# Optimization experiments

Measured on AMD Instinct MI355X. Metric: run time of the kernel, lower is better.

The kernel has to match this reference:

```python
import jax, jax.numpy as jnp
import numpy as np

X_SIZE = 1024
N_HEADS = 16
N_BASIS = 10
MAX_LEN = 4096
CACHE_KEEP_LEN = 4096
B = 8
T_NEW = 128
T_PREV = 4096
HEAD_DIM = X_SIZE // N_HEADS
LN_EPS = 1e-5


def setup_inputs() -> dict:
    key = jax.random.key(0)
    ks = jax.random.split(key, 9)
    def w(k, shape, s):
        return jax.random.normal(k, shape, dtype=jnp.float32) * s
    inv = 1.0 / np.sqrt(X_SIZE)
    return {
        "X": w(ks[0], (B, T_NEW, X_SIZE), 1.0),
        "cache_K": w(ks[1], (B, T_PREV, X_SIZE), 1.0),
        "cache_V": w(ks[2], (B, T_PREV, X_SIZE), 1.0),
        "Wq": w(ks[3], (X_SIZE, X_SIZE), 0.1 * inv),   # Q_SCALE=0.1 (NormedLinear init scale)
        "bq": jnp.zeros((X_SIZE,), jnp.float32),
        "Wk": w(ks[4], (X_SIZE, X_SIZE), 0.2 * inv),   # K_SCALE=0.2, no bias
        "Wv": w(ks[5], (X_SIZE, X_SIZE), 1.0 * inv),   # V_SCALE*sqrt(scale), no bias
        "Wproj": w(ks[6], (X_SIZE, X_SIZE), 1.0 * inv),
        "bproj": jnp.zeros((X_SIZE,), jnp.float32),
        "Wr": w(ks[7], (X_SIZE, N_BASIS * N_HEADS), 0.1 * inv),  # R_SCALE=0.1
        "br": jnp.zeros((N_BASIS * N_HEADS,), jnp.float32),
        "b_nd": w(ks[8], (N_BASIS, MAX_LEN), 0.2),     # B_SCALE=0.2
        "ln_g": jnp.ones((X_SIZE,), jnp.float32),
        "ln_b": jnp.zeros((X_SIZE,), jnp.float32),
    }


def _split_heads(x, h):
    b, t, e = x.shape
    return x.reshape(b, t, h, e // h).transpose(0, 2, 1, 3).reshape(b * h, t, e // h)


def _merge_heads(x, h):
    bh, t, q = x.shape
    b = bh // h
    return x.reshape(b, h, t, q).transpose(0, 2, 1, 3).reshape(b, t, h * q)


def reference(X, cache_K, cache_V, Wq, bq, Wk, Wv, Wproj, bproj, Wr, br, b_nd, ln_g, ln_b):
    Bsz, t, E = X.shape
    # ln_x
    mu = jnp.mean(X, axis=-1, keepdims=True)
    var = jnp.var(X, axis=-1, keepdims=True)
    Xn = (X - mu) / jnp.sqrt(var + LN_EPS) * ln_g + ln_b
    # projections on new tokens
    Q = Xn @ Wq + bq
    K_new = Xn @ Wk
    V_new = Xn @ Wv
    # update_state: append cache (startfull=max(Tprev-cache_keep_len,0))
    Tprev = cache_K.shape[1]
    start = max(Tprev - CACHE_KEEP_LEN, 0)
    Kf = jnp.concatenate([cache_K[:, start:], K_new], axis=1)  # (B, T, E)
    Vf = jnp.concatenate([cache_V[:, start:], V_new], axis=1)
    T = Kf.shape[1]
    Qh = _split_heads(Q, N_HEADS)   # (B*h, t, q)
    Kh = _split_heads(Kf, N_HEADS)  # (B*h, T, q)
    Vh = _split_heads(Vf, N_HEADS)
    # relattn logits: R_btn (B*h, t, n_basis), bandified basis D_ntT
    R = _split_heads(Xn @ Wr + br, N_HEADS)
    d = (T - t + jnp.arange(t)[:, None]) - jnp.arange(T)[None, :]  # (t, T) time diff
    valid = (d >= 0) & (d < MAX_LEN)
    D = jnp.where(valid[None, :, :], b_nd[:, jnp.clip(d, 0, MAX_LEN - 1)], 0.0)  # (n, t, T)
    extra = jnp.einsum('btn,ntT->btT', R, D)  # (B*h, t, T)
    # causal band bias (mask=None -> default causal mask with maxlen window)
    bias = jnp.where(valid, 0.0, -1e9)[None, :, :]
    logits = bias + extra + jnp.einsum('btq,bTq->btT', Qh, Kh) * (1.0 / np.sqrt(HEAD_DIM))
    W_btT = jax.nn.softmax(logits, axis=-1)
    A = _merge_heads(jnp.einsum('btT,bTq->btq', W_btT, Vh), N_HEADS)  # (B, t, E)
    return X + (A @ Wproj + bproj)
```

## Files before the change

kernel.cpp:

```cpp
#include <hip/hip_runtime.h>
#include <hip/hip_bf16.h>

typedef __bf16 bf16;
typedef __bf16 bf16x8 __attribute__((ext_vector_type(8)));
typedef float f32x4 __attribute__((ext_vector_type(4)));
typedef unsigned short u16;
typedef u16 u16x4 __attribute__((ext_vector_type(4)));

#define MFMA16(a, b, c) __builtin_amdgcn_mfma_f32_16x16x32_bf16(a, b, c, 0, 0, 0)

static __device__ __forceinline__ bf16x8 cvt8(float4 a, float4 b) {
  union { bf16 h[8]; bf16x8 v; } u;
  u.h[0] = (bf16)a.x; u.h[1] = (bf16)a.y; u.h[2] = (bf16)a.z; u.h[3] = (bf16)a.w;
  u.h[4] = (bf16)b.x; u.h[5] = (bf16)b.y; u.h[6] = (bf16)b.z; u.h[7] = (bf16)b.w;
  return u.v;
}

__global__ __launch_bounds__(256) void k_ln(const float* __restrict__ X,
                                            const float* __restrict__ g,
                                            const float* __restrict__ bb,
                                            bf16* __restrict__ Xn) {
  int m = blockIdx.x, t = threadIdx.x;
  const float* row = X + (size_t)m * 1024;
  float4 x = ((const float4*)row)[t];
  float s1 = x.x + x.y + x.z + x.w;
  float s2 = x.x * x.x + x.y * x.y + x.z * x.z + x.w * x.w;
#pragma unroll
  for (int off = 1; off < 64; off <<= 1) {
    s1 += __shfl_xor(s1, off);
    s2 += __shfl_xor(s2, off);
  }
  __shared__ float ws1[4], ws2[4];
  int w = t >> 6;
  if ((t & 63) == 0) { ws1[w] = s1; ws2[w] = s2; }
  __syncthreads();
  s1 = ws1[0] + ws1[1] + ws1[2] + ws1[3];
  s2 = ws2[0] + ws2[1] + ws2[2] + ws2[3];
  float mu = s1 * (1.f / 1024.f);
  float var = s2 * (1.f / 1024.f) - mu * mu;
  float rstd = rsqrtf(var + 1e-5f);
  float4 gg = ((const float4*)g)[t];
  float4 bv = ((const float4*)bb)[t];
  union { bf16 h[4]; u16x4 v; } u;
  u.h[0] = (bf16)((x.x - mu) * rstd * gg.x + bv.x);
  u.h[1] = (bf16)((x.y - mu) * rstd * gg.y + bv.y);
  u.h[2] = (bf16)((x.z - mu) * rstd * gg.z + bv.z);
  u.h[3] = (bf16)((x.w - mu) * rstd * gg.w + bv.w);
  ((u16x4*)(Xn + (size_t)m * 1024))[t] = u.v;
}

__global__ __launch_bounds__(256) void k_convert(const float* __restrict__ Wq,
                                                 const float* __restrict__ Wk,
                                                 const float* __restrict__ Wv,
                                                 const float* __restrict__ Wr,
                                                 const float* __restrict__ Wp,
                                                 bf16* __restrict__ Wt_all,
                                                 bf16* __restrict__ Wpt) {
  __shared__ float tile[64][65];
  int t = threadIdx.x;
  int bn = blockIdx.x / 16, bk = blockIdx.x % 16;
  int n0 = bn * 64, k0 = bk * 64;
#pragma unroll
  for (int it = 0; it < 16; ++it) {
    int idx = t + 256 * it;
    int kl = idx >> 6, nl = idx & 63;
    int n = n0 + nl, k = k0 + kl;
    float v;
    if (n < 1024)       v = Wq[(size_t)k * 1024 + n];
    else if (n < 2048)  v = Wk[(size_t)k * 1024 + (n - 1024)];
    else if (n < 3072)  v = Wv[(size_t)k * 1024 + (n - 2048)];
    else if (n < 3232)  v = Wr[(size_t)k * 160 + (n - 3072)];
    else if (n < 3328)  v = 0.f;
    else                v = Wp[(size_t)k * 1024 + (n - 3328)];
    tile[kl][nl] = v;
  }
  __syncthreads();
#pragma unroll
  for (int it = 0; it < 16; ++it) {
    int idx = t + 256 * it;
    int nl = idx >> 6, kl = idx & 63;
    int n = n0 + nl, k = k0 + kl;
    bf16 v = (bf16)tile[kl][nl];
    if (n < 3328) Wt_all[(size_t)n * 1024 + k] = v;
    else          Wpt[(size_t)(n - 3328) * 1024 + k] = v;
  }
}

template <int MODE>
__global__ __launch_bounds__(256) void k_gemm(const bf16* __restrict__ A,
                                              const bf16* __restrict__ Bw,
                                              bf16* __restrict__ Qb, bf16* __restrict__ Kn,
                                              bf16* __restrict__ Vn, float* __restrict__ Rws,
                                              const float* __restrict__ bq,
                                              const float* __restrict__ br,
                                              float* __restrict__ Out,
                                              const float* __restrict__ bproj,
                                              const float* __restrict__ Xres) {
  __shared__ __align__(16) bf16 As[128][72];
  __shared__ __align__(16) bf16 Bs[128][72];
  int t = threadIdx.x, l = t & 63, wid = t >> 6;
  int ln = l & 15, grp = l >> 4;
  int m0 = blockIdx.y * 128, n0 = blockIdx.x * 128;
  int wr = wid >> 1, wc = wid & 1;
  f32x4 acc[4][4] = {};
  int srow = t >> 1, shalf = (t & 1) * 32;

  for (int kt = 0; kt < 16; ++kt) {
    int k0 = kt * 64;
    const bf16* asrc = A + (size_t)(m0 + srow) * 1024 + k0 + shalf;
    const bf16* bsrc = Bw + (size_t)(n0 + srow) * 1024 + k0 + shalf;
    bf16x8 a0 = ((const bf16x8*)asrc)[0], a1 = ((const bf16x8*)asrc)[1];
    bf16x8 a2 = ((const bf16x8*)asrc)[2], a3 = ((const bf16x8*)asrc)[3];
    bf16x8 b0 = ((const bf16x8*)bsrc)[0], b1 = ((const bf16x8*)bsrc)[1];
    bf16x8 b2 = ((const bf16x8*)bsrc)[2], b3 = ((const bf16x8*)bsrc)[3];
    __syncthreads();
    *(bf16x8*)&As[srow][shalf + 0] = a0;  *(bf16x8*)&As[srow][shalf + 8] = a1;
    *(bf16x8*)&As[srow][shalf + 16] = a2; *(bf16x8*)&As[srow][shalf + 24] = a3;
    *(bf16x8*)&Bs[srow][shalf + 0] = b0;  *(bf16x8*)&Bs[srow][shalf + 8] = b1;
    *(bf16x8*)&Bs[srow][shalf + 16] = b2; *(bf16x8*)&Bs[srow][shalf + 24] = b3;
    __syncthreads();
#pragma unroll
    for (int ks = 0; ks < 2; ++ks) {
      int kk = ks * 32 + grp * 8;
      bf16x8 af[4], bf[4];
#pragma unroll
      for (int is = 0; is < 4; ++is) af[is] = *(const bf16x8*)&As[wr * 64 + is * 16 + ln][kk];
#pragma unroll
      for (int js = 0; js < 4; ++js) bf[js] = *(const bf16x8*)&Bs[wc * 64 + js * 16 + ln][kk];
#pragma unroll
      for (int is = 0; is < 4; ++is)
#pragma unroll
        for (int js = 0; js < 4; ++js) acc[is][js] = MFMA16(af[is], bf[js], acc[is][js]);
    }
  }

#pragma unroll
  for (int is = 0; is < 4; ++is)
#pragma unroll
    for (int js = 0; js < 4; ++js)
#pragma unroll
      for (int r = 0; r < 4; ++r) {
        int m = m0 + wr * 64 + is * 16 + grp * 4 + r;
        int n = n0 + wc * 64 + js * 16 + ln;
        float v = acc[is][js][r];
        if (MODE == 0) {
          int b = m >> 7, il = m & 127;
          if (n < 1024) {
            int h = n >> 6, dm = n & 63;
            Qb[((size_t)(b * 16 + h) * 128 + il) * 64 + dm] = (bf16)((v + bq[n]) * 0.125f);
          } else if (n < 2048) {
            Kn[(size_t)m * 1024 + (n - 1024)] = (bf16)v;
          } else if (n < 3072) {
            Vn[(size_t)m * 1024 + (n - 2048)] = (bf16)v;
          } else if (n < 3232) {
            int e = n - 3072, hh = e / 10, nb = e - hh * 10;
            Rws[((size_t)(b * 16 + hh) * 128 + il) * 10 + nb] = v + br[e];
          }
        } else {
          Out[(size_t)m * 1024 + n] = v + bproj[n] + Xres[(size_t)m * 1024 + n];
        }
      }
}

__global__ __launch_bounds__(512, 4) void k_attn(const float* __restrict__ cacheK,
                                                 const float* __restrict__ cacheV,
                                                 const bf16* __restrict__ Kn,
                                                 const bf16* __restrict__ Vn,
                                                 const bf16* __restrict__ Qb,
                                                 const float* __restrict__ Rws,
                                                 const float* __restrict__ bnd,
                                                 float* __restrict__ Opart,
                                                 float* __restrict__ mws,
                                                 float* __restrict__ lws) {
  __shared__ __align__(16) bf16 Ks[64][72];
  __shared__ __align__(16) bf16 Vt[64][72];
  __shared__ __align__(16) bf16 Gw[8][80][20];
  __shared__ __align__(16) bf16 bT[192][16];

  int t = threadIdx.x, l = t & 63, w = t >> 6;
  int grp = l >> 4, ln = l & 15;
  int s = blockIdx.x % 6, bh = blockIdx.x / 6;
  int b = bh >> 4, h = bh & 15;

  if (t < 192) {
#pragma unroll
    for (int e = 10; e < 16; ++e) bT[t][e] = (bf16)0.f;
  }

  int iq = w * 16 + ln;
  bf16x8 qf[2];
  qf[0] = *(const bf16x8*)(Qb + ((size_t)bh * 128 + iq) * 64 + grp * 8);
  qf[1] = *(const bf16x8*)(Qb + ((size_t)bh * 128 + iq) * 64 + 32 + grp * 8);
  bf16x8 rf;
  {
    union { bf16 hh[8]; bf16x8 v; } u;
    const float* rrow = Rws + ((size_t)bh * 128 + iq) * 10;
#pragma unroll
    for (int e = 0; e < 8; ++e) {
      int k = grp * 8 + e;
      u.hh[e] = (bf16)(k < 10 ? rrow[k] : 0.f);
    }
    rf = u.v;
  }

  int krow = t >> 3, kcb = (t & 7) * 8;
  int vjl = t & 63, vd0 = (t >> 6) * 8;
  int bc = t >> 1, bnh = (t & 1) * 5;

  float4 kA, kB, vA, vB;
  float bnv[5];

  auto issue = [&](int jt0) {
    if (jt0 < 4096) {
      const float* src = cacheK + ((size_t)(b * 4096 + jt0 + krow)) * 1024 + h * 64 + kcb;
      kA = *(const float4*)src;
      kB = *(const float4*)(src + 4);
      const float* sv = cacheV + ((size_t)(b * 4096 + jt0 + vjl)) * 1024 + h * 64 + vd0;
      vA = *(const float4*)sv;
      vB = *(const float4*)(sv + 4);
    } else {
      bf16x8 kN = *(const bf16x8*)(Kn + ((size_t)(b * 128 + (jt0 + krow - 4096))) * 1024 + h * 64 + kcb);
      bf16x8 vN = *(const bf16x8*)(Vn + ((size_t)(b * 128 + (jt0 + vjl - 4096))) * 1024 + h * 64 + vd0);
      kA = make_float4((float)kN[0], (float)kN[1], (float)kN[2], (float)kN[3]);
      kB = make_float4((float)kN[4], (float)kN[5], (float)kN[6], (float)kN[7]);
      vA = make_float4((float)vN[0], (float)vN[1], (float)vN[2], (float)vN[3]);
      vB = make_float4((float)vN[4], (float)vN[5], (float)vN[6], (float)vN[7]);
    }
    if (t < 384) {
      int d = (4033 - jt0) + bc;
      d = d < 0 ? 0 : (d > 4095 ? 4095 : d);
#pragma unroll
      for (int k = 0; k < 5; ++k) bnv[k] = bnd[(size_t)(bnh + k) * 4096 + d];
    }
  };

  issue(s * 704);

  f32x4 Oacc[4] = {};
  float m_r[4], l_r[4];
#pragma unroll
  for (int r = 0; r < 4; ++r) { m_r[r] = -1e30f; l_r[r] = 0.f; }

  for (int tt = 0; tt < 11; ++tt) {
    int jt0 = s * 704 + tt * 64;
    __syncthreads();
    *(bf16x8*)&Ks[krow][kcb] = cvt8(kA, kB);
    Vt[vd0 + 0][vjl] = (bf16)vA.x; Vt[vd0 + 1][vjl] = (bf16)vA.y;
    Vt[vd0 + 2][vjl] = (bf16)vA.z; Vt[vd0 + 3][vjl] = (bf16)vA.w;
    Vt[vd0 + 4][vjl] = (bf16)vB.x; Vt[vd0 + 5][vjl] = (bf16)vB.y;
    Vt[vd0 + 6][vjl] = (bf16)vB.z; Vt[vd0 + 7][vjl] = (bf16)vB.w;
    if (t < 384) {
#pragma unroll
      for (int k = 0; k < 5; ++k) bT[bc][bnh + k] = (bf16)bnv[k];
    }
    __syncthreads();
    if (tt + 1 < 11) issue(jt0 + 64);

    __builtin_amdgcn_s_setprio(1);
    f32x4 Sacc[4] = {};
#pragma unroll
    for (int ks = 0; ks < 2; ++ks) {
      int kk = ks * 32 + grp * 8;
#pragma unroll
      for (int js = 0; js < 4; ++js) {
        bf16x8 bfr = *(const bf16x8*)&Ks[js * 16 + ln][kk];
        Sacc[js] = MFMA16(qf[ks], bfr, Sacc[js]);
      }
    }
#pragma unroll
    for (int u = 0; u < 5; ++u) {
      bf16x8 bfr = *(const bf16x8*)&bT[(w + u) * 16 + ln][grp * 8];
      f32x4 z = {};
      f32x4 g = MFMA16(rf, bfr, z);
      union { bf16 hh[4]; u16x4 v; } uu;
      uu.hh[0] = (bf16)g[0]; uu.hh[1] = (bf16)g[1];
      uu.hh[2] = (bf16)g[2]; uu.hh[3] = (bf16)g[3];
      *(u16x4*)&Gw[w][u * 16 + ln][grp * 4] = uu.v;
    }
    __builtin_amdgcn_s_setprio(0);

#pragma unroll
    for (int r = 0; r < 4; ++r) {
      int irow = grp * 4 + r;
      int il = w * 16 + irow;
#pragma unroll
      for (int js = 0; js < 4; ++js) {
        int jj = js * 16 + ln;
        int d = 4096 + il - (jt0 + jj);
        bool valid = ((unsigned)d) < 4096u;
        int cl = 63 + irow - jj;
        float g = (float)Gw[w][cl][irow];
        Sacc[js][r] = valid ? (Sacc[js][r] + g) : -1e9f;
      }
    }
    bf16* Pw = (bf16*)&Gw[w][0][0];
#pragma unroll
    for (int r = 0; r < 4; ++r) {
      int irow = grp * 4 + r;
      float mx = fmaxf(fmaxf(Sacc[0][r], Sacc[1][r]), fmaxf(Sacc[2][r], Sacc[3][r]));
#pragma unroll
      for (int off = 1; off < 16; off <<= 1) mx = fmaxf(mx, __shfl_xor(mx, off));
      float mnew = fmaxf(m_r[r], mx);
      float sc = __expf(m_r[r] - mnew);
      m_r[r] = mnew;
      float rs = 0.f;
#pragma unroll
      for (int js = 0; js < 4; ++js) {
        float p = __expf(Sacc[js][r] - mnew);
        rs += p;
        Pw[irow * 72 + js * 16 + ln] = (bf16)p;
      }
#pragma unroll
      for (int off = 1; off < 16; off <<= 1) rs += __shfl_xor(rs, off);
      l_r[r] = l_r[r] * sc + rs;
#pragma unroll
      for (int ds = 0; ds < 4; ++ds) Oacc[ds][r] *= sc;
    }

    __builtin_amdgcn_s_setprio(1);
    {
      bf16x8 pa0 = *(const bf16x8*)&Pw[ln * 72 + grp * 8];
      bf16x8 pa1 = *(const bf16x8*)&Pw[ln * 72 + 32 + grp * 8];
#pragma unroll
      for (int ds = 0; ds < 4; ++ds) {
        bf16x8 v0 = *(const bf16x8*)&Vt[ds * 16 + ln][grp * 8];
        bf16x8 v1 = *(const bf16x8*)&Vt[ds * 16 + ln][32 + grp * 8];
        Oacc[ds] = MFMA16(pa0, v0, Oacc[ds]);
        Oacc[ds] = MFMA16(pa1, v1, Oacc[ds]);
      }
    }
    __builtin_amdgcn_s_setprio(0);
  }

  int part = s * 128 + bh;
#pragma unroll
  for (int ds = 0; ds < 4; ++ds)
#pragma unroll
    for (int r = 0; r < 4; ++r) {
      int il = w * 16 + grp * 4 + r;
      Opart[((size_t)part * 128 + il) * 64 + ds * 16 + ln] = Oacc[ds][r];
    }
  if (ln == 0) {
#pragma unroll
    for (int r = 0; r < 4; ++r) {
      int il = w * 16 + grp * 4 + r;
      mws[(size_t)part * 128 + il] = m_r[r];
      lws[(size_t)part * 128 + il] = l_r[r];
    }
  }
}

__global__ __launch_bounds__(256) void k_combine(const float* __restrict__ Opart,
                                                 const float* __restrict__ mws,
                                                 const float* __restrict__ lws,
                                                 bf16* __restrict__ Aout) {
  int bh = blockIdx.x, q = blockIdx.y, t = threadIdx.x;
  int dm = t & 63, iq = t >> 6;
  int b = bh >> 4, h = bh & 15;
  for (int ii = 0; ii < 8; ++ii) {
    int i = q * 32 + iq * 8 + ii;
    float ms[6], M = -1e30f;
#pragma unroll
    for (int s = 0; s < 6; ++s) {
      ms[s] = mws[(size_t)(s * 128 + bh) * 128 + i];
      M = fmaxf(M, ms[s]);
    }
    float L = 0.f, acc = 0.f;
#pragma unroll
    for (int s = 0; s < 6; ++s) {
      float wgt = __expf(ms[s] - M);
      L += wgt * lws[(size_t)(s * 128 + bh) * 128 + i];
      acc += wgt * Opart[((size_t)(s * 128 + bh) * 128 + i) * 64 + dm];
    }
    Aout[((size_t)(b * 128 + i)) * 1024 + h * 64 + dm] = (bf16)(acc / L);
  }
}

extern "C" void kernel_launch(void* const* d_in, const int* in_sizes, int n_in,
                              void* d_out, int out_size, void* d_ws, size_t ws_size,
                              hipStream_t stream) {
  (void)in_sizes; (void)n_in; (void)out_size; (void)ws_size;
  const float* X      = (const float*)d_in[0];
  const float* cacheK = (const float*)d_in[1];
  const float* cacheV = (const float*)d_in[2];
  const float* Wq     = (const float*)d_in[3];
  const float* bq     = (const float*)d_in[4];
  const float* Wk     = (const float*)d_in[5];
  const float* Wv     = (const float*)d_in[6];
  const float* Wproj  = (const float*)d_in[7];
  const float* bproj  = (const float*)d_in[8];
  const float* Wr     = (const float*)d_in[9];
  const float* br     = (const float*)d_in[10];
  const float* bnd    = (const float*)d_in[11];
  const float* lng    = (const float*)d_in[12];
  const float* lnb    = (const float*)d_in[13];
  float* out = (float*)d_out;

  char* ws = (char*)d_ws;
  bf16* Wt_all = (bf16*)ws;  ws += (size_t)3328 * 1024 * 2;
  bf16* Wpt    = (bf16*)ws;  ws += (size_t)1024 * 1024 * 2;
  bf16* Xn     = (bf16*)ws;  ws += (size_t)1024 * 1024 * 2;
  bf16* Qb     = (bf16*)ws;  ws += (size_t)1024 * 1024 * 2;
  bf16* Kn     = (bf16*)ws;  ws += (size_t)1024 * 1024 * 2;
  bf16* Vn     = (bf16*)ws;  ws += (size_t)1024 * 1024 * 2;
  bf16* Aattn  = (bf16*)ws;  ws += (size_t)1024 * 1024 * 2;
  float* Rws   = (float*)ws; ws += (size_t)128 * 128 * 10 * 4;
  float* mws   = (float*)ws; ws += (size_t)6 * 128 * 128 * 4;
  float* lws   = (float*)ws; ws += (size_t)6 * 128 * 128 * 4;
  float* Opart = (float*)ws; ws += (size_t)6 * 128 * 128 * 64 * 4;

  k_convert<<<dim3(68 * 16), 256, 0, stream>>>(Wq, Wk, Wv, Wr, Wproj, Wt_all, Wpt);
  k_ln<<<dim3(1024), 256, 0, stream>>>(X, lng, lnb, Xn);
  k_gemm<0><<<dim3(26, 8), 256, 0, stream>>>(Xn, Wt_all, Qb, Kn, Vn, Rws, bq, br,
                                             nullptr, nullptr, nullptr);
  k_attn<<<dim3(768), 512, 0, stream>>>(cacheK, cacheV, Kn, Vn, Qb, Rws, bnd,
                                        Opart, mws, lws);
  k_combine<<<dim3(128, 4), 256, 0, stream>>>(Opart, mws, lws, Aattn);
  k_gemm<1><<<dim3(8, 8), 256, 0, stream>>>(Aattn, Wpt, nullptr, nullptr, nullptr,
                                            nullptr, nullptr, nullptr, out, bproj, X);
}
```

Measured before the change: 190.1 us.

## Double-buffer attention K/V tiles, double split-K count, store partials in bf16

The attention kernel now keeps two LDS buffers for K, V and the basis tile. Each iteration writes the next tile into the spare buffer while the current one is consumed, which removes one barrier per iteration. The key range is split into 12 chunks per head instead of 6, giving 1536 blocks. Partial outputs are stored as bf16 to halve combine traffic, at some precision cost. The extra LDS may reduce occupancy, and the combine kernel now has to merge twice as many partials.

New measurement: 216.2 us. +13.7%, slower.

```diff
diff --git a/kernel.cpp b/kernel.cpp
--- a/kernel.cpp
+++ b/kernel.cpp
@@ -169,22 +169,25 @@
                                                  const bf16* __restrict__ Qb,
                                                  const float* __restrict__ Rws,
                                                  const float* __restrict__ bnd,
-                                                 float* __restrict__ Opart,
+                                                 bf16* __restrict__ Opart,
                                                  float* __restrict__ mws,
                                                  float* __restrict__ lws) {
-  __shared__ __align__(16) bf16 Ks[64][72];
-  __shared__ __align__(16) bf16 Vt[64][72];
+  __shared__ __align__(16) bf16 Ks[2][64][72];
+  __shared__ __align__(16) bf16 Vt[2][64][72];
   __shared__ __align__(16) bf16 Gw[8][80][20];
-  __shared__ __align__(16) bf16 bT[192][16];
+  __shared__ __align__(16) bf16 bT[2][192][16];
 
   int t = threadIdx.x, l = t & 63, w = t >> 6;
   int grp = l >> 4, ln = l & 15;
-  int s = blockIdx.x % 6, bh = blockIdx.x / 6;
+  int s = blockIdx.x % 12, bh = blockIdx.x / 12;
   int b = bh >> 4, h = bh & 15;
+  int toff = s < 6 ? s * 6 : 36 + (s - 6) * 5;
+  int nt   = s < 6 ? 6 : 5;
+  int jbase = toff * 64;
 
   if (t < 192) {
 #pragma unroll
-    for (int e = 10; e < 16; ++e) bT[t][e] = (bf16)0.f;
+    for (int e = 10; e < 16; ++e) { bT[0][t][e] = (bf16)0.f; bT[1][t][e] = (bf16)0.f; }
   }
 
   int iq = w * 16 + ln;
@@ -233,28 +236,33 @@
       for (int k = 0; k < 5; ++k) bnv[k] = bnd[(size_t)(bnh + k) * 4096 + d];
     }
   };
-
-  issue(s * 704);
+  auto stage = [&](int p) {
+    *(bf16x8*)&Ks[p][krow][kcb] = cvt8(kA, kB);
+    Vt[p][vd0 + 0][vjl] = (bf16)vA.x; Vt[p][vd0 + 1][vjl] = (bf16)vA.y;
+    Vt[p][vd0 + 2][vjl] = (bf16)vA.z; Vt[p][vd0 + 3][vjl] = (bf16)vA.w;
+    Vt[p][vd0 + 4][vjl] = (bf16)vB.x; Vt[p][vd0 + 5][vjl] = (bf16)vB.y;
+    Vt[p][vd0 + 6][vjl] = (bf16)vB.z; Vt[p][vd0 + 7][vjl] = (bf16)vB.w;
+    if (t < 384) {
+#pragma unroll
+      for (int k = 0; k < 5; ++k) bT[p][bc][bnh + k] = (bf16)bnv[k];
+    }
+  };
+
+  issue(jbase);
+  stage(0);
+  issue(jbase + 64);
 
   f32x4 Oacc[4] = {};
   float m_r[4], l_r[4];
 #pragma unroll
   for (int r = 0; r < 4; ++r) { m_r[r] = -1e30f; l_r[r] = 0.f; }
 
-  for (int tt = 0; tt < 11; ++tt) {
-    int jt0 = s * 704 + tt * 64;
+  for (int tt = 0; tt < nt; ++tt) {
+    int jt0 = jbase + tt * 64;
+    int cur = tt & 1;
     __syncthreads();
-    *(bf16x8*)&Ks[krow][kcb] = cvt8(kA, kB);
-    Vt[vd0 + 0][vjl] = (bf16)vA.x; Vt[vd0 + 1][vjl] = (bf16)vA.y;
-    Vt[vd0 + 2][vjl] = (bf16)vA.z; Vt[vd0 + 3][vjl] = (bf16)vA.w;
-    Vt[vd0 + 4][vjl] = (bf16)vB.x; Vt[vd0 + 5][vjl] = (bf16)vB.y;
-    Vt[vd0 + 6][vjl] = (bf16)vB.z; Vt[vd0 + 7][vjl] = (bf16)vB.w;
-    if (t < 384) {
-#pragma unroll
-      for (int k = 0; k < 5; ++k) bT[bc][bnh + k] = (bf16)bnv[k];
-    }
-    __syncthreads();
-    if (tt + 1 < 11) issue(jt0 + 64);
+    if (tt + 1 < nt) stage(cur ^ 1);
+    if (tt + 2 < nt) issue(jbase + (tt + 2) * 64);
 
     __builtin_amdgcn_s_setprio(1);
     f32x4 Sacc[4] = {};
@@ -263,13 +271,13 @@
       int kk = ks * 32 + grp * 8;
 #pragma unroll
       for (int js = 0; js < 4; ++js) {
-        bf16x8 bfr = *(const bf16x8*)&Ks[js * 16 + ln][kk];
+        bf16x8 bfr = *(const bf16x8*)&Ks[cur][js * 16 + ln][kk];
         Sacc[js] = MFMA16(qf[ks], bfr, Sacc[js]);
       }
     }
 #pragma unroll
     for (int u = 0; u < 5; ++u) {
-      bf16x8 bfr = *(const bf16x8*)&bT[(w + u) * 16 + ln][grp * 8];
+      bf16x8 bfr = *(const bf16x8*)&bT[cur][(w + u) * 16 + ln][grp * 8];
       f32x4 z = {};
       f32x4 g = MFMA16(rf, bfr, z);
       union { bf16 hh[4]; u16x4 v; } uu;
@@ -323,8 +331,8 @@
       bf16x8 pa1 = *(const bf16x8*)&Pw[ln * 72 + 32 + grp * 8];
 #pragma unroll
       for (int ds = 0; ds < 4; ++ds) {
-        bf16x8 v0 = *(const bf16x8*)&Vt[ds * 16 + ln][grp * 8];
-        bf16x8 v1 = *(const bf16x8*)&Vt[ds * 16 + ln][32 + grp * 8];
+        bf16x8 v0 = *(const bf16x8*)&Vt[cur][ds * 16 + ln][grp * 8];
+        bf16x8 v1 = *(const bf16x8*)&Vt[cur][ds * 16 + ln][32 + grp * 8];
         Oacc[ds] = MFMA16(pa0, v0, Oacc[ds]);
         Oacc[ds] = MFMA16(pa1, v1, Oacc[ds]);
       }
@@ -338,7 +346,7 @@
 #pragma unroll
     for (int r = 0; r < 4; ++r) {
       int il = w * 16 + grp * 4 + r;
-      Opart[((size_t)part * 128 + il) * 64 + ds * 16 + ln] = Oacc[ds][r];
+      Opart[((size_t)part * 128 + il) * 64 + ds * 16 + ln] = (bf16)Oacc[ds][r];
     }
   if (ln == 0) {
 #pragma unroll
@@ -350,7 +358,7 @@
   }
 }
 
-__global__ __launch_bounds__(256) void k_combine(const float* __restrict__ Opart,
+__global__ __launch_bounds__(256) void k_combine(const bf16* __restrict__ Opart,
                                                  const float* __restrict__ mws,
                                                  const float* __restrict__ lws,
                                                  bf16* __restrict__ Aout) {
@@ -359,18 +367,18 @@
   int b = bh >> 4, h = bh & 15;
   for (int ii = 0; ii < 8; ++ii) {
     int i = q * 32 + iq * 8 + ii;
-    float ms[6], M = -1e30f;
-#pragma unroll
-    for (int s = 0; s < 6; ++s) {
+    float ms[12], M = -1e30f;
+#pragma unroll
+    for (int s = 0; s < 12; ++s) {
       ms[s] = mws[(size_t)(s * 128 + bh) * 128 + i];
       M = fmaxf(M, ms[s]);
     }
     float L = 0.f, acc = 0.f;
 #pragma unroll
-    for (int s = 0; s < 6; ++s) {
+    for (int s = 0; s < 12; ++s) {
       float wgt = __expf(ms[s] - M);
       L += wgt * lws[(size_t)(s * 128 + bh) * 128 + i];
-      acc += wgt * Opart[((size_t)(s * 128 + bh) * 128 + i) * 64 + dm];
+      acc += wgt * (float)Opart[((size_t)(s * 128 + bh) * 128 + i) * 64 + dm];
     }
     Aout[((size_t)(b * 128 + i)) * 1024 + h * 64 + dm] = (bf16)(acc / L);
   }
@@ -405,16 +413,16 @@
   bf16* Vn     = (bf16*)ws;  ws += (size_t)1024 * 1024 * 2;
   bf16* Aattn  = (bf16*)ws;  ws += (size_t)1024 * 1024 * 2;
   float* Rws   = (float*)ws; ws += (size_t)128 * 128 * 10 * 4;
-  float* mws   = (float*)ws; ws += (size_t)6 * 128 * 128 * 4;
-  float* lws   = (float*)ws; ws += (size_t)6 * 128 * 128 * 4;
-  float* Opart = (float*)ws; ws += (size_t)6 * 128 * 128 * 64 * 4;
+  float* mws   = (float*)ws; ws += (size_t)12 * 128 * 128 * 4;
+  float* lws   = (float*)ws; ws += (size_t)12 * 128 * 128 * 4;
+  bf16* Opart  = (bf16*)ws;  ws += (size_t)12 * 128 * 128 * 64 * 2;
 
   k_convert<<<dim3(68 * 16), 256, 0, stream>>>(Wq, Wk, Wv, Wr, Wproj, Wt_all, Wpt);
   k_ln<<<dim3(1024), 256, 0, stream>>>(X, lng, lnb, Xn);
   k_gemm<0><<<dim3(26, 8), 256, 0, stream>>>(Xn, Wt_all, Qb, Kn, Vn, Rws, bq, br,
                                              nullptr, nullptr, nullptr);
-  k_attn<<<dim3(768), 512, 0, stream>>>(cacheK, cacheV, Kn, Vn, Qb, Rws, bnd,
-                                        Opart, mws, lws);
+  k_attn<<<dim3(1536), 512, 0, stream>>>(cacheK, cacheV, Kn, Vn, Qb, Rws, bnd,
+                                         Opart, mws, lws);
   k_combine<<<dim3(128, 4), 256, 0, stream>>>(Opart, mws, lws, Aattn);
   k_gemm<1><<<dim3(8, 8), 256, 0, stream>>>(Aattn, Wpt, nullptr, nullptr, nullptr,
                                             nullptr, nullptr, nullptr, out, bproj, X);
```
